# Kernel tuning notes

Hardware: AMD Instinct MI355X
Metric: run time of the kernel (lower is better)

Reference implementation:

```python
import jax, jax.numpy as jnp
import numpy as np

N_CLASSES = 21


def setup_inputs() -> dict:
    key = jax.random.key(0)
    k1, k2 = jax.random.split(key)
    pred = jax.random.normal(k1, (16, N_CLASSES, 512, 512), dtype=jnp.float32)
    gt = jax.random.randint(k2, (16, 1, 512, 512), 0, N_CLASSES, dtype=jnp.int32)
    return {"pred": pred, "gt": gt}


def reference(pred, gt):
    # pred: [B, C, H, W] logits; gt: [B, 1, H, W] int class ids
    C = pred.shape[1]
    pm = jnp.argmax(pred, axis=1).reshape(-1)          # flattened predicted class per pixel
    gm = gt.reshape(-1).astype(pm.dtype)
    match = (pm == gm).astype(jnp.float32)
    inter = jnp.bincount(pm, weights=match, length=C)                  # |pred==c & gt==c|
    cp = jnp.bincount(pm, length=C).astype(jnp.float32)                # |pred==c|
    cg = jnp.bincount(gm, length=C).astype(jnp.float32)                # |gt==c|
    union = cp + cg - inter                                            # |pred==c | gt==c|
    # original: iou = 0 when intersection == 0 (also guards union == 0)
    iou = jnp.where(inter > 0, inter / jnp.where(union > 0, union, 1.0), 0.0)
    return jnp.mean(iou)  # sum over C classes / N_CLASSES
```

## Files before the change

kernel.cpp:

```cpp
#include <hip/hip_runtime.h>

#define NCLS 21
#define HW   (512 * 512)
#define NB   16
#define NPIX (NB * HW)
#define BLK  1024
#define SEG  8192
#define CHUNK 4096
#define GRID (NPIX / SEG)

typedef float v4f __attribute__((ext_vector_type(4)));
typedef int   v4i __attribute__((ext_vector_type(4)));

__global__ void __launch_bounds__(BLK) iou_hist_kernel(
    const float* __restrict__ pred, const int* __restrict__ gt,
    unsigned int* __restrict__ cnt) {
    __shared__ unsigned int h[3 * NCLS];
    for (int i = threadIdx.x; i < 3 * NCLS; i += BLK) h[i] = 0u;
    __syncthreads();

    const int p0 = blockIdx.x * SEG + threadIdx.x * 4;
    const int b  = p0 >> 18;
    const int hw = p0 & (HW - 1);
    const float* base = pred + (size_t)b * (NCLS * HW) + hw;

    v4f mA = *(const v4f*)base;
    v4f mB = *(const v4f*)(base + CHUNK);
    int a0 = 0, a1 = 0, a2 = 0, a3 = 0;
    int b0 = 0, b1 = 0, b2 = 0, b3 = 0;
#pragma unroll
    for (int c = 1; c < NCLS; ++c) {
        const float* pc = base + (size_t)c * HW;
        const v4f xA = *(const v4f*)pc;
        const v4f xB = *(const v4f*)(pc + CHUNK);
        if (xA.x > mA.x) { mA.x = xA.x; a0 = c; }
        if (xA.y > mA.y) { mA.y = xA.y; a1 = c; }
        if (xA.z > mA.z) { mA.z = xA.z; a2 = c; }
        if (xA.w > mA.w) { mA.w = xA.w; a3 = c; }
        if (xB.x > mB.x) { mB.x = xB.x; b0 = c; }
        if (xB.y > mB.y) { mB.y = xB.y; b1 = c; }
        if (xB.z > mB.z) { mB.z = xB.z; b2 = c; }
        if (xB.w > mB.w) { mB.w = xB.w; b3 = c; }
    }
    const v4i gA = *(const v4i*)(gt + p0);
    const v4i gB = *(const v4i*)(gt + p0 + CHUNK);

    atomicAdd(&h[NCLS + a0], 1u);
    atomicAdd(&h[NCLS + a1], 1u);
    atomicAdd(&h[NCLS + a2], 1u);
    atomicAdd(&h[NCLS + a3], 1u);
    atomicAdd(&h[NCLS + b0], 1u);
    atomicAdd(&h[NCLS + b1], 1u);
    atomicAdd(&h[NCLS + b2], 1u);
    atomicAdd(&h[NCLS + b3], 1u);
    atomicAdd(&h[2 * NCLS + gA.x], 1u);
    atomicAdd(&h[2 * NCLS + gA.y], 1u);
    atomicAdd(&h[2 * NCLS + gA.z], 1u);
    atomicAdd(&h[2 * NCLS + gA.w], 1u);
    atomicAdd(&h[2 * NCLS + gB.x], 1u);
    atomicAdd(&h[2 * NCLS + gB.y], 1u);
    atomicAdd(&h[2 * NCLS + gB.z], 1u);
    atomicAdd(&h[2 * NCLS + gB.w], 1u);
    if (a0 == gA.x) atomicAdd(&h[a0], 1u);
    if (a1 == gA.y) atomicAdd(&h[a1], 1u);
    if (a2 == gA.z) atomicAdd(&h[a2], 1u);
    if (a3 == gA.w) atomicAdd(&h[a3], 1u);
    if (b0 == gB.x) atomicAdd(&h[b0], 1u);
    if (b1 == gB.y) atomicAdd(&h[b1], 1u);
    if (b2 == gB.z) atomicAdd(&h[b2], 1u);
    if (b3 == gB.w) atomicAdd(&h[b3], 1u);

    __syncthreads();
    for (int i = threadIdx.x; i < 3 * NCLS; i += BLK) {
        unsigned int val = h[i];
        if (val) atomicAdd(&cnt[i], val);
    }
}

__global__ void iou_final_kernel(const unsigned int* __restrict__ cnt,
                                 float* __restrict__ out) {
    const int lane = threadIdx.x;
    float iou = 0.0f;
    if (lane < NCLS) {
        const float inter = (float)cnt[lane];
        const float cp    = (float)cnt[NCLS + lane];
        const float cg    = (float)cnt[2 * NCLS + lane];
        const float uni   = cp + cg - inter;
        iou = (inter > 0.0f) ? inter / (uni > 0.0f ? uni : 1.0f) : 0.0f;
    }
#pragma unroll
    for (int off = 32; off >= 1; off >>= 1)
        iou += __shfl_down(iou, off, 64);
    if (lane == 0) out[0] = iou / (float)NCLS;
}

extern "C" void kernel_launch(void* const* d_in, const int* in_sizes, int n_in,
                              void* d_out, int out_size, void* d_ws, size_t ws_size,
                              hipStream_t stream) {
    const float*  pred = (const float*)d_in[0];
    const int*    gt   = (const int*)d_in[1];
    float*        out  = (float*)d_out;
    unsigned int* cnt  = (unsigned int*)d_ws;

    hipMemsetAsync(cnt, 0, 3 * NCLS * sizeof(unsigned int), stream);

    iou_hist_kernel<<<GRID, BLK, 0, stream>>>(pred, gt, cnt);
    iou_final_kernel<<<1, 64, 0, stream>>>(cnt, out);
}
```

Baseline: 75.12 us.

## Replace global atomics with per-block partial histograms reduced in final kernel

Each histogram block now writes its 63 shared counts to a private strided slot in the workspace, instead of doing atomicAdds on one global histogram. The final kernel runs 1024 threads; 16 groups each sum 32 blocks' partials per slot, then combine through shared atomics before computing IoU. The hipMemsetAsync is removed because every slot is overwritten. This removes contention on the global atomics and one memset launch, at the cost of a serial reduction over 512 partials in a single-block final kernel.

```diff
diff --git a/kernel.cpp b/kernel.cpp
--- a/kernel.cpp
+++ b/kernel.cpp
@@ -8,6 +8,7 @@
 #define SEG  8192
 #define CHUNK 4096
 #define GRID (NPIX / SEG)
+#define CSTRIDE 64
 
 typedef float v4f __attribute__((ext_vector_type(4)));
 typedef int   v4i __attribute__((ext_vector_type(4)));
@@ -71,27 +72,41 @@
     if (b3 == gB.w) atomicAdd(&h[b3], 1u);
 
     __syncthreads();
-    for (int i = threadIdx.x; i < 3 * NCLS; i += BLK) {
-        unsigned int val = h[i];
-        if (val) atomicAdd(&cnt[i], val);
-    }
+    unsigned int* myout = cnt + (size_t)blockIdx.x * CSTRIDE;
+    for (int i = threadIdx.x; i < 3 * NCLS; i += BLK)
+        myout[i] = h[i];
 }
 
-__global__ void iou_final_kernel(const unsigned int* __restrict__ cnt,
-                                 float* __restrict__ out) {
-    const int lane = threadIdx.x;
+__global__ void __launch_bounds__(1024) iou_final_kernel(
+    const unsigned int* __restrict__ cnt, float* __restrict__ out) {
+    __shared__ unsigned int tot[3 * NCLS];
+    if (threadIdx.x < 3 * NCLS) tot[threadIdx.x] = 0u;
+    __syncthreads();
+
+    const int slot = threadIdx.x & 63;
+    const int g    = threadIdx.x >> 6;
+    if (slot < 3 * NCLS) {
+        unsigned int s = 0;
+        const int blk0 = g * (GRID / 16);
+#pragma unroll 4
+        for (int kb = blk0; kb < blk0 + GRID / 16; ++kb)
+            s += cnt[(size_t)kb * CSTRIDE + slot];
+        atomicAdd(&tot[slot], s);
+    }
+    __syncthreads();
+
     float iou = 0.0f;
-    if (lane < NCLS) {
-        const float inter = (float)cnt[lane];
-        const float cp    = (float)cnt[NCLS + lane];
-        const float cg    = (float)cnt[2 * NCLS + lane];
+    if (threadIdx.x < NCLS) {
+        const float inter = (float)tot[threadIdx.x];
+        const float cp    = (float)tot[NCLS + threadIdx.x];
+        const float cg    = (float)tot[2 * NCLS + threadIdx.x];
         const float uni   = cp + cg - inter;
         iou = (inter > 0.0f) ? inter / (uni > 0.0f ? uni : 1.0f) : 0.0f;
     }
 #pragma unroll
     for (int off = 32; off >= 1; off >>= 1)
         iou += __shfl_down(iou, off, 64);
-    if (lane == 0) out[0] = iou / (float)NCLS;
+    if (threadIdx.x == 0) out[0] = iou / (float)NCLS;
 }
 
 extern "C" void kernel_launch(void* const* d_in, const int* in_sizes, int n_in,
@@ -102,8 +117,6 @@
     float*        out  = (float*)d_out;
     unsigned int* cnt  = (unsigned int*)d_ws;
 
-    hipMemsetAsync(cnt, 0, 3 * NCLS * sizeof(unsigned int), stream);
-
     iou_hist_kernel<<<GRID, BLK, 0, stream>>>(pred, gt, cnt);
-    iou_final_kernel<<<1, 64, 0, stream>>>(cnt, out);
+    iou_final_kernel<<<1, 1024, 0, stream>>>(cnt, out);
 }
```

Result: faster. 69.06 us, median of 2 (-8.1%).
